# Kernel tuning notes

Measured on AMD Instinct MI355X. Metric: run time of the kernel, lower is better.

## Reference

```python
import jax, jax.numpy as jnp
import numpy as np

N = 50000   # nodes
E = 800000  # edges
IN, H1, H2, OUT = 128, 256, 128, 1


def setup_inputs() -> dict:
    key = jax.random.key(0)
    ks = jax.random.split(key, 9)
    x = jax.random.normal(ks[0], (N, IN), dtype=jnp.float32)
    edge_index = jax.random.randint(ks[1], (2, E), 0, N, dtype=jnp.int32)
    def glorot(k, fan_in, fan_out):
        s = np.sqrt(6.0 / (fan_in + fan_out)).astype(np.float32)
        return jax.random.uniform(k, (fan_in, fan_out), jnp.float32, -s, s)
    W1 = glorot(ks[2], IN, H1)
    b1 = jnp.zeros((H1,), jnp.float32)
    W2 = glorot(ks[3], H1, H2)
    b2 = jnp.zeros((H2,), jnp.float32)
    W3 = glorot(ks[4], H2, OUT)
    b3 = jnp.zeros((OUT,), jnp.float32)
    return {"x": x, "edge_index": edge_index, "W1": W1, "b1": b1,
            "W2": W2, "b2": b2, "W3": W3, "b3": b3}


def _gcn_layer(x, W, b, src, dst, norm):
    # dense transform [N, d_in] @ [d_in, d_out]
    h = x @ W
    # degree-normalized sparse aggregation: out[dst] += norm * h[src]
    agg = jax.ops.segment_sum(h[src] * norm[:, None], dst, num_segments=N)
    return agg + b


def reference(x, edge_index, W1, b1, W2, b2, W3, b3):
    src, dst = edge_index[0], edge_index[1]
    # PyG GCNConv: add self loops, then symmetric normalization
    loop = jnp.arange(N, dtype=src.dtype)
    src = jnp.concatenate([src, loop])
    dst = jnp.concatenate([dst, loop])
    deg = jax.ops.segment_sum(jnp.ones_like(dst, jnp.float32), dst, num_segments=N)
    dis = jax.lax.rsqrt(jnp.maximum(deg, 1.0))  # deg >= 1 via self loops
    norm = dis[src] * dis[dst]  # [E+N]
    h1 = jax.nn.relu(_gcn_layer(x, W1, b1, src, dst, norm))
    h2 = jax.nn.relu(_gcn_layer(h1, W2, b2, src, dst, norm))
    y = _gcn_layer(h2, W3, b3, src, dst, norm).reshape(-1)
    return (y, h1, h2)
```

## Files before the change

### kernel.cpp

```cpp
#include <hip/hip_runtime.h>


typedef __attribute__((ext_vector_type(8))) short short8;
typedef __attribute__((ext_vector_type(4))) float f32x4;

static __device__ __forceinline__ unsigned short f2bf(float f){
  union { float f; unsigned u; } v; v.f = f;
  unsigned r = v.u + 0x7FFF + ((v.u >> 16) & 1);
  return (unsigned short)(r >> 16);
}
static __device__ __forceinline__ float2 bf2f2(unsigned u){
  union { unsigned u; float f; } a, b;
  a.u = u << 16; b.u = u & 0xffff0000u;
  return make_float2(a.f, b.f);
}

__global__ __launch_bounds__(256) void k_prepbin(
    const int* __restrict__ src, const int* __restrict__ dst,
    int* __restrict__ bcur, unsigned* __restrict__ pairs, int E, int binB,
    const float* __restrict__ W1, const float* __restrict__ W2,
    unsigned short* __restrict__ Wf1, unsigned short* __restrict__ Wf2,
    const float4* __restrict__ x, uint2* __restrict__ xb, int nv){
  __shared__ int cl[256];
  int blk = blockIdx.x;
  int tid = threadIdx.x;
  if (blk < binB){
    int e0 = blk * 4096 + tid;
    cl[tid] = 0; __syncthreads();
    #pragma unroll
    for (int i = 0; i < 16; i++){
      int e = e0 + i*256;
      if (e < E) atomicAdd(&cl[dst[e] >> 8], 1);
    }
    __syncthreads();
    int c = cl[tid];
    int g = (c > 0) ? atomicAdd(&bcur[tid], c) : 0;
    cl[tid] = g;
    __syncthreads();
    #pragma unroll
    for (int i = 0; i < 16; i++){
      int e = e0 + i*256;
      if (e < E){
        int d = dst[e];
        int b = d >> 8;
        int p = atomicAdd(&cl[b], 1);
        pairs[(b << 13) + p] = (unsigned)src[e] | ((unsigned)(d & 255) << 16);
      }
    }
  } else if (blk < binB + 256){
    int t = (blk - binB)*256 + tid;
    if (t < 32768){
      int j = t & 7, lane = (t>>3) & 63, kt = (t>>9) & 3, nt = t >> 11;
      int nn = nt*16 + (lane & 15);
      int kk = kt*32 + (lane>>4)*8 + j;
      Wf1[t] = f2bf(W1[kk*256 + nn]);
    } else {
      int o = t - 32768;
      int j = o & 7, lane = (o>>3) & 63, ntl = (o>>9) & 3, kt = (o>>11) & 7, h = o >> 14;
      int nn = (h*4 + ntl)*16 + (lane & 15);
      int kk = kt*32 + (lane>>4)*8 + j;
      Wf2[o] = f2bf(W2[kk*128 + nn]);
    }
  } else {
    int i = (blk - binB - 256)*256 + tid;
    if (i < nv){
      float4 v = x[i];
      xb[i] = make_uint2((unsigned)f2bf(v.x) | ((unsigned)f2bf(v.y) << 16),
                         (unsigned)f2bf(v.z) | ((unsigned)f2bf(v.w) << 16));
    }
  }
}

__global__ __launch_bounds__(256) void k_place(
    const int* __restrict__ bcur, const unsigned* __restrict__ pairs,
    unsigned short* __restrict__ csr_src, int* __restrict__ rowptr,
    int* __restrict__ cnt, float* __restrict__ dis, int n, int nb){
  __shared__ int sh[256];
  __shared__ int ncnt[256];
  int t = threadIdx.x;
  int b = blockIdx.x;
  int v = (t < nb) ? bcur[t] : 0;
  sh[t] = v; __syncthreads();
  for (int off = 1; off < 256; off <<= 1){
    int x = (t >= off) ? sh[t-off] : 0;
    __syncthreads(); sh[t] += x; __syncthreads();
  }
  int csr_base = (b == 0) ? 0 : sh[b-1];
  int cnt_b = bcur[b];
  ncnt[t] = 0; __syncthreads();
  const unsigned* P = pairs + ((size_t)b << 13);
  for (int i = t; i < cnt_b; i += 256) atomicAdd(&ncnt[P[i] >> 16], 1);
  __syncthreads();
  int c = ncnt[t];
  sh[t] = c; __syncthreads();
  for (int off = 1; off < 256; off <<= 1){
    int x = (t >= off) ? sh[t-off] : 0;
    __syncthreads(); sh[t] += x; __syncthreads();
  }
  int noff = sh[t] - c;
  int node = (b << 8) + t;
  if (node < n){
    rowptr[node] = csr_base + noff;
    cnt[node] = c;
    dis[node] = rsqrtf((float)(c + 1));
  }
  ncnt[t] = noff; __syncthreads();
  for (int i = t; i < cnt_b; i += 256){
    unsigned u = P[i];
    int p = atomicAdd(&ncnt[u >> 16], 1);
    csr_src[csr_base + p] = (unsigned short)(u & 0xffff);
  }
}

__global__ void k_aggL1(const unsigned* __restrict__ xb, unsigned* __restrict__ out,
                        const int* __restrict__ rowptr, const int* __restrict__ cnt,
                        const unsigned short* __restrict__ csr_src,
                        const float* __restrict__ dis, int n){
  int t = threadIdx.x;
  int lane = t & 63;
  int node = blockIdx.x*4 + (t >> 6);
  if (node >= n) return;
  float di = dis[node];
  float2 v = bf2f2(xb[(size_t)node*64 + lane]);
  float2 acc = make_float2(di*v.x, di*v.y);
  int start = rowptr[node];
  int mm = cnt[node];
  int j = 0;
  for (; j + 15 < mm; j += 16){
    int s[16]; unsigned uv[16]; float w[16];
    #pragma unroll
    for (int q = 0; q < 16; q++) s[q] = csr_src[start+j+q];
    #pragma unroll
    for (int q = 0; q < 16; q++){ w[q] = dis[s[q]]; uv[q] = xb[(size_t)s[q]*64 + lane]; }
    #pragma unroll
    for (int q = 0; q < 16; q++){
      float2 u = bf2f2(uv[q]);
      acc.x = fmaf(w[q], u.x, acc.x); acc.y = fmaf(w[q], u.y, acc.y);
    }
  }
  for (; j + 3 < mm; j += 4){
    int s[4]; unsigned uv[4]; float w[4];
    #pragma unroll
    for (int q = 0; q < 4; q++) s[q] = csr_src[start+j+q];
    #pragma unroll
    for (int q = 0; q < 4; q++){ w[q] = dis[s[q]]; uv[q] = xb[(size_t)s[q]*64 + lane]; }
    #pragma unroll
    for (int q = 0; q < 4; q++){
      float2 u = bf2f2(uv[q]);
      acc.x = fmaf(w[q], u.x, acc.x); acc.y = fmaf(w[q], u.y, acc.y);
    }
  }
  for (; j < mm; j++){
    int s = csr_src[start+j];
    float2 u = bf2f2(xb[(size_t)s*64 + lane]);
    float w = dis[s];
    acc.x = fmaf(w, u.x, acc.x); acc.y = fmaf(w, u.y, acc.y);
  }
  acc.x *= di; acc.y *= di;
  out[(size_t)node*64 + lane] =
      (unsigned)f2bf(acc.x) | ((unsigned)f2bf(acc.y) << 16);
}

__global__ void k_aggL2(const unsigned* __restrict__ t2b, float* __restrict__ h2,
                        const int* __restrict__ rowptr, const int* __restrict__ cnt,
                        const unsigned short* __restrict__ csr_src,
                        const float* __restrict__ dis,
                        const float* __restrict__ b2, const float* __restrict__ W3,
                        float* __restrict__ u, int n){
  int t = threadIdx.x;
  int lane = t & 63;
  int node = blockIdx.x*4 + (t >> 6);
  if (node >= n) return;
  float di = dis[node];
  float2 v = bf2f2(t2b[(size_t)node*64 + lane]);
  float2 acc = make_float2(di*v.x, di*v.y);
  int start = rowptr[node];
  int mm = cnt[node];
  int j = 0;
  for (; j + 15 < mm; j += 16){
    int s[16]; unsigned uv[16]; float w[16];
    #pragma unroll
    for (int q = 0; q < 16; q++) s[q] = csr_src[start+j+q];
    #pragma unroll
    for (int q = 0; q < 16; q++){ w[q] = dis[s[q]]; uv[q] = t2b[(size_t)s[q]*64 + lane]; }
    #pragma unroll
    for (int q = 0; q < 16; q++){
      float2 uu = bf2f2(uv[q]);
      acc.x = fmaf(w[q], uu.x, acc.x); acc.y = fmaf(w[q], uu.y, acc.y);
    }
  }
  for (; j + 3 < mm; j += 4){
    int s[4]; unsigned uv[4]; float w[4];
    #pragma unroll
    for (int q = 0; q < 4; q++) s[q] = csr_src[start+j+q];
    #pragma unroll
    for (int q = 0; q < 4; q++){ w[q] = dis[s[q]]; uv[q] = t2b[(size_t)s[q]*64 + lane]; }
    #pragma unroll
    for (int q = 0; q < 4; q++){
      float2 uu = bf2f2(uv[q]);
      acc.x = fmaf(w[q], uu.x, acc.x); acc.y = fmaf(w[q], uu.y, acc.y);
    }
  }
  for (; j < mm; j++){
    int s = csr_src[start+j];
    float2 uu = bf2f2(t2b[(size_t)s*64 + lane]);
    float w = dis[s];
    acc.x = fmaf(w, uu.x, acc.x); acc.y = fmaf(w, uu.y, acc.y);
  }
  float2 b = ((const float2*)b2)[lane];
  acc.x = fmaxf(fmaf(di, acc.x, b.x), 0.0f);
  acc.y = fmaxf(fmaf(di, acc.y, b.y), 0.0f);
  ((float2*)h2)[(size_t)node*64 + lane] = acc;
  float up = fmaf(acc.x, W3[2*lane], acc.y * W3[2*lane+1]);
  #pragma unroll
  for (int off = 32; off > 0; off >>= 1) up += __shfl_down(up, off);
  if (lane == 0) u[node] = up;
}

__global__ __launch_bounds__(256) void k_gemm1_mfma(
    const unsigned short* __restrict__ Xa, const unsigned short* __restrict__ Wf1,
    const float* __restrict__ bias, float* __restrict__ out,
    unsigned short* __restrict__ h1b, int n)
{
  __shared__ unsigned short Wl[8*4*64*8];
  int t = threadIdx.x;
  int row0 = (blockIdx.x >> 1) * 64;
  int h = blockIdx.x & 1;
  int w = t >> 6, lane = t & 63, m = lane & 15, q = lane >> 4;
  int rbase = w*16;
  int rowm = row0 + rbase + m;
  int ra = (rowm < n) ? rowm : (n-1);
  const short8* Arow = (const short8*)(Xa + (size_t)ra*128);
  short8 af[4];
  #pragma unroll
  for (int kt = 0; kt < 4; kt++) af[kt] = Arow[kt*4 + q];
  {
    const float4* src = (const float4*)Wf1 + (size_t)h*2048;
    float4* dst = (float4*)Wl;
    #pragma unroll
    for (int i = 0; i < 8; i++) dst[i*256 + t] = src[i*256 + t];
  }
  __syncthreads();
  f32x4 acc[8];
  #pragma unroll
  for (int i = 0; i < 8; i++) acc[i] = (f32x4){0.f,0.f,0.f,0.f};
  const short8* Wv = (const short8*)Wl;
  #pragma unroll
  for (int nt = 0; nt < 8; nt++){
    #pragma unroll
    for (int kt = 0; kt < 4; kt++){
      short8 bfr = Wv[(nt*4 + kt)*64 + lane];
      acc[nt] = __builtin_amdgcn_mfma_f32_16x16x32_bf16(af[kt], bfr, acc[nt], 0, 0, 0);
    }
  }
  int rowa = row0 + rbase + q*4;
  int colb = h*128 + m;
  #pragma unroll
  for (int nt = 0; nt < 8; nt++){
    float b = bias[colb + nt*16];
    #pragma unroll
    for (int r = 0; r < 4; r++){
      int rr = rowa + r;
      if (rr < n){
        float o = fmaxf(acc[nt][r] + b, 0.0f);
        out[(size_t)rr*256 + colb + nt*16] = o;
        h1b[(size_t)rr*256 + colb + nt*16] = f2bf(o);
      }
    }
  }
}

__global__ __launch_bounds__(256) void k_gemm2_mfma(
    const unsigned short* __restrict__ H1b, const unsigned short* __restrict__ Wf2,
    unsigned short* __restrict__ T2b, int n)
{
  __shared__ unsigned short Wl[32*64*8];
  int t = threadIdx.x;
  int row0 = (blockIdx.x >> 1) * 64;
  int h = blockIdx.x & 1;
  int w = t >> 6, lane = t & 63, m = lane & 15, q = lane >> 4;
  int rbase = w*16;
  int rowm = row0 + rbase + m;
  int ra = (rowm < n) ? rowm : (n-1);
  const short8* Arow = (const short8*)(H1b + (size_t)ra*256);
  short8 af[8];
  #pragma unroll
  for (int kt = 0; kt < 8; kt++) af[kt] = Arow[kt*4 + q];
  {
    const float4* src = (const float4*)Wf2 + (size_t)h*2048;
    float4* dst = (float4*)Wl;
    #pragma unroll
    for (int i = 0; i < 8; i++) dst[i*256 + t] = src[i*256 + t];
  }
  __syncthreads();
  f32x4 acc[4];
  #pragma unroll
  for (int i = 0; i < 4; i++) acc[i] = (f32x4){0.f,0.f,0.f,0.f};
  const short8* Wv = (const short8*)Wl;
  #pragma unroll
  for (int nt = 0; nt < 4; nt++){
    #pragma unroll
    for (int kt = 0; kt < 8; kt++){
      short8 bfr = Wv[(kt*4 + nt)*64 + lane];
      acc[nt] = __builtin_amdgcn_mfma_f32_16x16x32_bf16(af[kt], bfr, acc[nt], 0, 0, 0);
    }
  }
  int rowa = row0 + rbase + q*4;
  #pragma unroll
  for (int nt = 0; nt < 4; nt++){
    int col = h*64 + nt*16 + m;
    #pragma unroll
    for (int r = 0; r < 4; r++){
      int rr = rowa + r;
      if (rr < n) T2b[(size_t)rr*128 + col] = f2bf(acc[nt][r]);
    }
  }
}

__global__ void k_agg1d(const float* __restrict__ u, float* __restrict__ y,
                        const int* __restrict__ rowptr, const int* __restrict__ cnt,
                        const unsigned short* __restrict__ csr_src,
                        const float* __restrict__ dis,
                        const float* __restrict__ b3, int n){
  int i = blockIdx.x*256 + threadIdx.x;
  if (i >= n) return;
  float di = dis[i];
  float acc = di * u[i];
  int s0 = rowptr[i], m = cnt[i];
  for (int j = 0; j < m; j++){
    int s = csr_src[s0+j];
    acc = fmaf(dis[s], u[s], acc);
  }
  y[i] = fmaf(di, acc, b3[0]);
}

extern "C" void kernel_launch(void* const* d_in, const int* in_sizes, int n_in,
                              void* d_out, int out_size, void* d_ws, size_t ws_size,
                              hipStream_t stream){
  const float* x  = (const float*)d_in[0];
  const int*  ei  = (const int*)d_in[1];
  const float* W1 = (const float*)d_in[2];
  const float* b1 = (const float*)d_in[3];
  const float* W2 = (const float*)d_in[4];
  const float* b2 = (const float*)d_in[5];
  const float* W3 = (const float*)d_in[6];
  const float* b3 = (const float*)d_in[7];
  const int N = in_sizes[0] / 128;
  const int E = in_sizes[1] / 2;
  const int* src = ei;
  const int* dst = ei + E;
  const int NB = (N + 255) >> 8;

  char* p = (char*)d_ws;
  auto alloc = [&](size_t bytes)->char*{
    char* r = p; p += (bytes + 255) & ~(size_t)255; return r;
  };
  int*   bcur    = (int*)  alloc(256*4);
  int*   rowptr  = (int*)  alloc((size_t)N*4);
  int*   cnt     = (int*)  alloc((size_t)N*4);
  float* dis     = (float*)alloc((size_t)N*4);
  unsigned* pairs = (unsigned*)alloc((size_t)NB*8192*4);
  unsigned short* csr_src = (unsigned short*)alloc((size_t)E*2);
  unsigned* xb   = (unsigned*)alloc((size_t)N*128*2);
  unsigned* xa   = (unsigned*)alloc((size_t)N*128*2);
  unsigned short* h1b = (unsigned short*)alloc((size_t)N*256*2);
  unsigned short* t2b = (unsigned short*)alloc((size_t)N*128*2);
  float* u       = (float*)alloc((size_t)N*4);
  unsigned short* wf1 = (unsigned short*)alloc(32768*2);
  unsigned short* wf2 = (unsigned short*)alloc(32768*2);

  float* y  = (float*)d_out;
  float* h1 = y + N;
  float* h2 = h1 + (size_t)N*256;

  int bb = (E + 4095)/4096;
  int nb = (N + 255)/256;
  int xv = N*32;
  int xblk = (xv + 255)/256;

  hipMemsetAsync(bcur, 0, 256*4, stream);
  k_prepbin <<<bb + 256 + xblk, 256, 0, stream>>>(
      src, dst, bcur, pairs, E, bb, W1, W2, wf1, wf2,
      (const float4*)x, (uint2*)xb, xv);
  k_place   <<<NB, 256, 0, stream>>>(bcur, pairs, csr_src, rowptr, cnt, dis, N, NB);

  int ab = (N + 3)/4;
  int rb = (N + 63)/64;
  k_aggL1     <<<ab,   256, 0, stream>>>(xb, xa, rowptr, cnt, csr_src, dis, N);
  k_gemm1_mfma<<<rb*2, 256, 0, stream>>>((const unsigned short*)xa, wf1, b1, h1, h1b, N);
  k_gemm2_mfma<<<rb*2, 256, 0, stream>>>(h1b, wf2, t2b, N);
  k_aggL2     <<<ab,   256, 0, stream>>>((const unsigned*)t2b, h2, rowptr, cnt, csr_src, dis, b2, W3, u, N);
  k_agg1d     <<<nb,   256, 0, stream>>>(u, y, rowptr, cnt, csr_src, dis, b3, N);
}
```

Measured before the change: 258.1 us.

## Pre-scale features by source degree norm and drop per-edge dis gathers

```diff
diff --git a/kernel.cpp b/kernel.cpp
--- a/kernel.cpp
+++ b/kernel.cpp
@@ -19,8 +19,7 @@
     const int* __restrict__ src, const int* __restrict__ dst,
     int* __restrict__ bcur, unsigned* __restrict__ pairs, int E, int binB,
     const float* __restrict__ W1, const float* __restrict__ W2,
-    unsigned short* __restrict__ Wf1, unsigned short* __restrict__ Wf2,
-    const float4* __restrict__ x, uint2* __restrict__ xb, int nv){
+    unsigned short* __restrict__ Wf1, unsigned short* __restrict__ Wf2){
   __shared__ int cl[256];
   int blk = blockIdx.x;
   int tid = threadIdx.x;
@@ -47,7 +46,7 @@
         pairs[(b << 13) + p] = (unsigned)src[e] | ((unsigned)(d & 255) << 16);
       }
     }
-  } else if (blk < binB + 256){
+  } else {
     int t = (blk - binB)*256 + tid;
     if (t < 32768){
       int j = t & 7, lane = (t>>3) & 63, kt = (t>>9) & 3, nt = t >> 11;
@@ -61,13 +60,6 @@
       int kk = kt*32 + (lane>>4)*8 + j;
       Wf2[o] = f2bf(W2[kk*128 + nn]);
     }
-  } else {
-    int i = (blk - binB - 256)*256 + tid;
-    if (i < nv){
-      float4 v = x[i];
-      xb[i] = make_uint2((unsigned)f2bf(v.x) | ((unsigned)f2bf(v.y) << 16),
-                         (unsigned)f2bf(v.z) | ((unsigned)f2bf(v.w) << 16));
-    }
   }
 }
 
@@ -112,7 +104,18 @@
   }
 }
 
-__global__ void k_aggL1(const unsigned* __restrict__ xb, unsigned* __restrict__ out,
+__global__ __launch_bounds__(256) void k_xscale(
+    const float4* __restrict__ x, const float* __restrict__ dis,
+    uint2* __restrict__ xbs, int n){
+  int i = blockIdx.x*256 + threadIdx.x;
+  if (i >= n*32) return;
+  float d = dis[i >> 5];
+  float4 v = x[i];
+  xbs[i] = make_uint2((unsigned)f2bf(d*v.x) | ((unsigned)f2bf(d*v.y) << 16),
+                      (unsigned)f2bf(d*v.z) | ((unsigned)f2bf(d*v.w) << 16));
+}
+
+__global__ void k_aggL1(const unsigned* __restrict__ xbs, unsigned* __restrict__ out,
                         const int* __restrict__ rowptr, const int* __restrict__ cnt,
                         const unsigned short* __restrict__ csr_src,
                         const float* __restrict__ dis, int n){
@@ -121,47 +124,43 @@
   int node = blockIdx.x*4 + (t >> 6);
   if (node >= n) return;
   float di = dis[node];
-  float2 v = bf2f2(xb[(size_t)node*64 + lane]);
-  float2 acc = make_float2(di*v.x, di*v.y);
+  float2 acc = bf2f2(xbs[(size_t)node*64 + lane]);
   int start = rowptr[node];
   int mm = cnt[node];
   int j = 0;
   for (; j + 15 < mm; j += 16){
-    int s[16]; unsigned uv[16]; float w[16];
+    int s[16]; unsigned uv[16];
     #pragma unroll
     for (int q = 0; q < 16; q++) s[q] = csr_src[start+j+q];
     #pragma unroll
-    for (int q = 0; q < 16; q++){ w[q] = dis[s[q]]; uv[q] = xb[(size_t)s[q]*64 + lane]; }
+    for (int q = 0; q < 16; q++) uv[q] = xbs[(size_t)s[q]*64 + lane];
     #pragma unroll
     for (int q = 0; q < 16; q++){
       float2 u = bf2f2(uv[q]);
-      acc.x = fmaf(w[q], u.x, acc.x); acc.y = fmaf(w[q], u.y, acc.y);
+      acc.x += u.x; acc.y += u.y;
     }
   }
   for (; j + 3 < mm; j += 4){
-    int s[4]; unsigned uv[4]; float w[4];
+    int s[4]; unsigned uv[4];
     #pragma unroll
     for (int q = 0; q < 4; q++) s[q] = csr_src[start+j+q];
     #pragma unroll
-    for (int q = 0; q < 4; q++){ w[q] = dis[s[q]]; uv[q] = xb[(size_t)s[q]*64 + lane]; }
+    for (int q = 0; q < 4; q++) uv[q] = xbs[(size_t)s[q]*64 + lane];
     #pragma unroll
     for (int q = 0; q < 4; q++){
       float2 u = bf2f2(uv[q]);
-      acc.x = fmaf(w[q], u.x, acc.x); acc.y = fmaf(w[q], u.y, acc.y);
+      acc.x += u.x; acc.y += u.y;
     }
   }
   for (; j < mm; j++){
-    int s = csr_src[start+j];
-    float2 u = bf2f2(xb[(size_t)s*64 + lane]);
-    float w = dis[s];
-    acc.x = fmaf(w, u.x, acc.x); acc.y = fmaf(w, u.y, acc.y);
-  }
-  acc.x *= di; acc.y *= di;
+    float2 u = bf2f2(xbs[(size_t)csr_src[start+j]*64 + lane]);
+    acc.x += u.x; acc.y += u.y;
+  }
   out[(size_t)node*64 + lane] =
-      (unsigned)f2bf(acc.x) | ((unsigned)f2bf(acc.y) << 16);
-}
-
-__global__ void k_aggL2(const unsigned* __restrict__ t2b, float* __restrict__ h2,
+      (unsigned)f2bf(di*acc.x) | ((unsigned)f2bf(di*acc.y) << 16);
+}
+
+__global__ void k_aggL2(const unsigned* __restrict__ t2s, float* __restrict__ h2,
                         const int* __restrict__ rowptr, const int* __restrict__ cnt,
                         const unsigned short* __restrict__ csr_src,
                         const float* __restrict__ dis,
@@ -172,40 +171,37 @@
   int node = blockIdx.x*4 + (t >> 6);
   if (node >= n) return;
   float di = dis[node];
-  float2 v = bf2f2(t2b[(size_t)node*64 + lane]);
-  float2 acc = make_float2(di*v.x, di*v.y);
+  float2 acc = bf2f2(t2s[(size_t)node*64 + lane]);
   int start = rowptr[node];
   int mm = cnt[node];
   int j = 0;
   for (; j + 15 < mm; j += 16){
-    int s[16]; unsigned uv[16]; float w[16];
+    int s[16]; unsigned uv[16];
     #pragma unroll
     for (int q = 0; q < 16; q++) s[q] = csr_src[start+j+q];
     #pragma unroll
-    for (int q = 0; q < 16; q++){ w[q] = dis[s[q]]; uv[q] = t2b[(size_t)s[q]*64 + lane]; }
+    for (int q = 0; q < 16; q++) uv[q] = t2s[(size_t)s[q]*64 + lane];
     #pragma unroll
     for (int q = 0; q < 16; q++){
       float2 uu = bf2f2(uv[q]);
-      acc.x = fmaf(w[q], uu.x, acc.x); acc.y = fmaf(w[q], uu.y, acc.y);
+      acc.x += uu.x; acc.y += uu.y;
     }
   }
   for (; j + 3 < mm; j += 4){
-    int s[4]; unsigned uv[4]; float w[4];
+    int s[4]; unsigned uv[4];
     #pragma unroll
     for (int q = 0; q < 4; q++) s[q] = csr_src[start+j+q];
     #pragma unroll
-    for (int q = 0; q < 4; q++){ w[q] = dis[s[q]]; uv[q] = t2b[(size_t)s[q]*64 + lane]; }
+    for (int q = 0; q < 4; q++) uv[q] = t2s[(size_t)s[q]*64 + lane];
     #pragma unroll
     for (int q = 0; q < 4; q++){
       float2 uu = bf2f2(uv[q]);
-      acc.x = fmaf(w[q], uu.x, acc.x); acc.y = fmaf(w[q], uu.y, acc.y);
+      acc.x += uu.x; acc.y += uu.y;
     }
   }
   for (; j < mm; j++){
-    int s = csr_src[start+j];
-    float2 uu = bf2f2(t2b[(size_t)s*64 + lane]);
-    float w = dis[s];
-    acc.x = fmaf(w, uu.x, acc.x); acc.y = fmaf(w, uu.y, acc.y);
+    float2 uu = bf2f2(t2s[(size_t)csr_src[start+j]*64 + lane]);
+    acc.x += uu.x; acc.y += uu.y;
   }
   float2 b = ((const float2*)b2)[lane];
   acc.x = fmaxf(fmaf(di, acc.x, b.x), 0.0f);
@@ -214,13 +210,12 @@
   float up = fmaf(acc.x, W3[2*lane], acc.y * W3[2*lane+1]);
   #pragma unroll
   for (int off = 32; off > 0; off >>= 1) up += __shfl_down(up, off);
-  if (lane == 0) u[node] = up;
+  if (lane == 0) u[node] = di * up;
 }
 
 __global__ __launch_bounds__(256) void k_gemm1_mfma(
     const unsigned short* __restrict__ Xa, const unsigned short* __restrict__ Wf1,
-    const float* __restrict__ bias, float* __restrict__ out,
-    unsigned short* __restrict__ h1b, int n)
+    const float* __restrict__ bias, float* __restrict__ out, int n)
 {
   __shared__ unsigned short Wl[8*4*64*8];
   int t = threadIdx.x;
@@ -261,18 +256,15 @@
     #pragma unroll
     for (int r = 0; r < 4; r++){
       int rr = rowa + r;
-      if (rr < n){
-        float o = fmaxf(acc[nt][r] + b, 0.0f);
-        out[(size_t)rr*256 + colb + nt*16] = o;
-        h1b[(size_t)rr*256 + colb + nt*16] = f2bf(o);
-      }
+      if (rr < n)
+        out[(size_t)rr*256 + colb + nt*16] = fmaxf(acc[nt][r] + b, 0.0f);
     }
   }
 }
 
 __global__ __launch_bounds__(256) void k_gemm2_mfma(
-    const unsigned short* __restrict__ H1b, const unsigned short* __restrict__ Wf2,
-    unsigned short* __restrict__ T2b, int n)
+    const float* __restrict__ H1, const unsigned short* __restrict__ Wf2,
+    const float* __restrict__ dis, unsigned short* __restrict__ T2s, int n)
 {
   __shared__ unsigned short Wl[32*64*8];
   int t = threadIdx.x;
@@ -282,10 +274,19 @@
   int rbase = w*16;
   int rowm = row0 + rbase + m;
   int ra = (rowm < n) ? rowm : (n-1);
-  const short8* Arow = (const short8*)(H1b + (size_t)ra*256);
+  const float4* Arow = (const float4*)(H1 + (size_t)ra*256);
   short8 af[8];
   #pragma unroll
-  for (int kt = 0; kt < 8; kt++) af[kt] = Arow[kt*4 + q];
+  for (int kt = 0; kt < 8; kt++){
+    float4 a0 = Arow[kt*8 + q*2];
+    float4 a1 = Arow[kt*8 + q*2 + 1];
+    short8 v;
+    v[0] = (short)f2bf(a0.x); v[1] = (short)f2bf(a0.y);
+    v[2] = (short)f2bf(a0.z); v[3] = (short)f2bf(a0.w);
+    v[4] = (short)f2bf(a1.x); v[5] = (short)f2bf(a1.y);
+    v[6] = (short)f2bf(a1.z); v[7] = (short)f2bf(a1.w);
+    af[kt] = v;
+  }
   {
     const float4* src = (const float4*)Wf2 + (size_t)h*2048;
     float4* dst = (float4*)Wl;
@@ -306,32 +307,40 @@
     }
   }
   int rowa = row0 + rbase + q*4;
+  float dsv[4];
+  #pragma unroll
+  for (int r = 0; r < 4; r++){
+    int rr = rowa + r;
+    dsv[r] = (rr < n) ? dis[rr] : 0.0f;
+  }
   #pragma unroll
   for (int nt = 0; nt < 4; nt++){
     int col = h*64 + nt*16 + m;
     #pragma unroll
     for (int r = 0; r < 4; r++){
       int rr = rowa + r;
-      if (rr < n) T2b[(size_t)rr*128 + col] = f2bf(acc[nt][r]);
-    }
-  }
-}
-
-__global__ void k_agg1d(const float* __restrict__ u, float* __restrict__ y,
+      if (rr < n) T2s[(size_t)rr*128 + col] = f2bf(dsv[r] * acc[nt][r]);
+    }
+  }
+}
+
+__global__ void k_agg1d(const float* __restrict__ us, float* __restrict__ y,
                         const int* __restrict__ rowptr, const int* __restrict__ cnt,
                         const unsigned short* __restrict__ csr_src,
                         const float* __restrict__ dis,
                         const float* __restrict__ b3, int n){
-  int i = blockIdx.x*256 + threadIdx.x;
-  if (i >= n) return;
-  float di = dis[i];
-  float acc = di * u[i];
-  int s0 = rowptr[i], m = cnt[i];
-  for (int j = 0; j < m; j++){
-    int s = csr_src[s0+j];
-    acc = fmaf(dis[s], u[s], acc);
-  }
-  y[i] = fmaf(di, acc, b3[0]);
+  int t = threadIdx.x;
+  int node = blockIdx.x*16 + (t >> 4);
+  int sub = t & 15;
+  if (node >= n) return;
+  int s0 = rowptr[node];
+  int m = cnt[node];
+  float acc = (sub == 0) ? us[node] : 0.0f;
+  for (int j = sub; j < m; j += 16)
+    acc += us[csr_src[s0 + j]];
+  #pragma unroll
+  for (int off = 8; off > 0; off >>= 1) acc += __shfl_xor(acc, off);
+  if (sub == 0) y[node] = fmaf(dis[node], acc, b3[0]);
 }
 
 extern "C" void kernel_launch(void* const* d_in, const int* in_sizes, int n_in,
@@ -361,10 +370,9 @@
   float* dis     = (float*)alloc((size_t)N*4);
   unsigned* pairs = (unsigned*)alloc((size_t)NB*8192*4);
   unsigned short* csr_src = (unsigned short*)alloc((size_t)E*2);
-  unsigned* xb   = (unsigned*)alloc((size_t)N*128*2);
+  unsigned* xbs  = (unsigned*)alloc((size_t)N*128*2);
   unsigned* xa   = (unsigned*)alloc((size_t)N*128*2);
-  unsigned short* h1b = (unsigned short*)alloc((size_t)N*256*2);
-  unsigned short* t2b = (unsigned short*)alloc((size_t)N*128*2);
+  unsigned short* t2s = (unsigned short*)alloc((size_t)N*128*2);
   float* u       = (float*)alloc((size_t)N*4);
   unsigned short* wf1 = (unsigned short*)alloc(32768*2);
   unsigned short* wf2 = (unsigned short*)alloc(32768*2);
@@ -374,21 +382,20 @@
   float* h2 = h1 + (size_t)N*256;
 
   int bb = (E + 4095)/4096;
-  int nb = (N + 255)/256;
-  int xv = N*32;
-  int xblk = (xv + 255)/256;
 
   hipMemsetAsync(bcur, 0, 256*4, stream);
-  k_prepbin <<<bb + 256 + xblk, 256, 0, stream>>>(
-      src, dst, bcur, pairs, E, bb, W1, W2, wf1, wf2,
-      (const float4*)x, (uint2*)xb, xv);
+  k_prepbin <<<bb + 256, 256, 0, stream>>>(
+      src, dst, bcur, pairs, E, bb, W1, W2, wf1, wf2);
   k_place   <<<NB, 256, 0, stream>>>(bcur, pairs, csr_src, rowptr, cnt, dis, N, NB);
+
+  int xq = N*32;
+  k_xscale  <<<(xq + 255)/256, 256, 0, stream>>>((const float4*)x, dis, (uint2*)xbs, N);
 
   int ab = (N + 3)/4;
   int rb = (N + 63)/64;
-  k_aggL1     <<<ab,   256, 0, stream>>>(xb, xa, rowptr, cnt, csr_src, dis, N);
-  k_gemm1_mfma<<<rb*2, 256, 0, stream>>>((const unsigned short*)xa, wf1, b1, h1, h1b, N);
-  k_gemm2_mfma<<<rb*2, 256, 0, stream>>>(h1b, wf2, t2b, N);
-  k_aggL2     <<<ab,   256, 0, stream>>>((const unsigned*)t2b, h2, rowptr, cnt, csr_src, dis, b2, W3, u, N);
-  k_agg1d     <<<nb,   256, 0, stream>>>(u, y, rowptr, cnt, csr_src, dis, b3, N);
-}
+  k_aggL1     <<<ab,   256, 0, stream>>>(xbs, xa, rowptr, cnt, csr_src, dis, N);
+  k_gemm1_mfma<<<rb*2, 256, 0, stream>>>((const unsigned short*)xa, wf1, b1, h1, N);
+  k_gemm2_mfma<<<rb*2, 256, 0, stream>>>(h1, wf2, dis, t2s, N);
+  k_aggL2     <<<ab,   256, 0, stream>>>((const unsigned*)t2s, h2, rowptr, cnt, csr_src, dis, b2, W3, u, N);
+  k_agg1d     <<<(N + 15)/16, 256, 0, stream>>>(u, y, rowptr, cnt, csr_src, dis, b3, N);
+}
```

After: 253.4 us. About the same (-1.8%).
